# Optimization experiments

Measured on AMD Instinct MI355X. Metric: run time of the kernel, lower is better.

The kernel has to match this reference:

```python
import jax, jax.numpy as jnp
import numpy as np

def setup_inputs() -> dict:
    key = jax.random.key(0)
    ks = jax.random.split(key, 8)
    B, C, H, W = 4, 64, 64, 64
    Cr = C // 8
    s = 1.0 / np.sqrt(C)
    return {
        "x": jax.random.normal(ks[0], (B, C, H, W), jnp.float32),
        "wq": jax.random.normal(ks[1], (Cr, C), jnp.float32) * s,
        "bq": jax.random.normal(ks[2], (Cr,), jnp.float32) * 0.01,
        "wk": jax.random.normal(ks[3], (Cr, C), jnp.float32) * s,
        "bk": jax.random.normal(ks[4], (Cr,), jnp.float32) * 0.01,
        "wv": jax.random.normal(ks[5], (C, C), jnp.float32) * s,
        "bv": jax.random.normal(ks[6], (C,), jnp.float32) * 0.01,
        "gamma": jax.random.normal(ks[7], (1,), jnp.float32) * 0.1,
    }

def reference(x, wq, bq, wk, bk, wv, bv, gamma):
    B, C, H, W = x.shape
    N = H * W
    xf = x.reshape(B, C, N)  # 1x1 conv == pointwise linear over channel dim
    q = jnp.einsum("oc,bcn->bno", wq, xf) + bq[None, None, :]   # (B, N, Cr)
    k = jnp.einsum("oc,bcn->bon", wk, xf) + bk[None, :, None]   # (B, Cr, N)
    v = jnp.einsum("oc,bcn->bon", wv, xf) + bv[None, :, None]   # (B, C, N)
    attn = jnp.einsum("bno,bom->bnm", q, k)                     # (B, N, N)
    attn = jax.nn.softmax(attn, axis=-1)
    out = jnp.einsum("bcm,bnm->bcn", v, attn)                   # (B, C, N)
    out = out.reshape(B, C, H, W)
    return x + gamma[0] * out
```

## Files before the change

### kernel.cpp

```cpp
#include <hip/hip_runtime.h>

#define BB 4
#define CC 64
#define NN 4096

typedef __attribute__((ext_vector_type(8)))  short short8;
typedef __attribute__((ext_vector_type(4)))  short short4v;
typedef __attribute__((ext_vector_type(4)))  float f32x4;
typedef __attribute__((ext_vector_type(16))) float f32x16;
typedef unsigned short u16;

#define QWS_ELEMS (BB * NN * 8)

__device__ inline u16 f2bf(float x) {
    unsigned u = __float_as_uint(x);
    u = (u + 0x7fffu + ((u >> 16) & 1u)) >> 16;
    return (u16)u;
}
__device__ inline unsigned pack2rne(float a, float b) {
    return (unsigned)f2bf(a) | ((unsigned)f2bf(b) << 16);
}
__device__ inline unsigned permpack(float lo, float hi) {
    return __builtin_amdgcn_perm(__float_as_uint(hi), __float_as_uint(lo), 0x07060302);
}

__device__ inline void barrier_lgkm() {
    asm volatile("s_waitcnt lgkmcnt(0)\n\ts_barrier" ::: "memory");
}

union SH8 {
    short8 s;
    struct Halves { short4v lo, hi; } h;
    uint4 u;
};

__global__ __launch_bounds__(512) void proj_kernel(
    const float* __restrict__ x,
    const float* __restrict__ wq, const float* __restrict__ bq,
    const float* __restrict__ wk, const float* __restrict__ bk,
    const float* __restrict__ wv, const float* __restrict__ bv,
    u16* __restrict__ ws_u)
{
    u16* qws = ws_u;
    u16* kws = ws_u + QWS_ELEMS;
    u16* vws = ws_u + 2 * QWS_ELEMS;

    const int y   = blockIdx.y;
    const int pix = blockIdx.x * 512 + threadIdx.x;
    const int b   = pix >> 12;
    const int n   = pix & (NN - 1);
    const float* xb = x + ((size_t)b << 18) + n;

    if (y < 8) {
        const int v0 = y << 3;
        float av[8];
#pragma unroll
        for (int i = 0; i < 8; ++i) av[i] = bv[v0 + i];
#pragma unroll 8
        for (int c = 0; c < CC; ++c) {
            const float xv = xb[(size_t)c << 12];
#pragma unroll
            for (int i = 0; i < 8; ++i)
                av[i] += wv[(v0 + i) * CC + c] * xv;
        }
#pragma unroll
        for (int i = 0; i < 8; ++i)
            vws[(((size_t)((b << 6) + v0 + i)) << 12) + n] = f2bf(av[i]);
    } else {
        float aq[8], ak[8];
#pragma unroll
        for (int i = 0; i < 8; ++i) { aq[i] = bq[i]; ak[i] = bk[i]; }
#pragma unroll 8
        for (int c = 0; c < CC; ++c) {
            const float xv = xb[(size_t)c << 12];
#pragma unroll
            for (int i = 0; i < 8; ++i) {
                aq[i] += wq[i * CC + c] * xv;
                ak[i] += wk[i * CC + c] * xv;
            }
        }
        uint4 qp, kp;
        qp.x = pack2rne(aq[0], aq[1]); qp.y = pack2rne(aq[2], aq[3]);
        qp.z = pack2rne(aq[4], aq[5]); qp.w = pack2rne(aq[6], aq[7]);
        kp.x = pack2rne(ak[0], ak[1]); kp.y = pack2rne(ak[2], ak[3]);
        kp.z = pack2rne(ak[4], ak[5]); kp.w = pack2rne(ak[6], ak[7]);
        *(uint4*)&qws[(size_t)pix * 8] = qp;
        *(uint4*)&kws[(size_t)pix * 8] = kp;
    }
}

__global__ __launch_bounds__(512) void attn_kernel(
    const float* __restrict__ x, const float* __restrict__ gamma,
    const u16* __restrict__ ws_u, float* __restrict__ out)
{
    const u16* qws = ws_u;
    const u16* kws = ws_u + QWS_ELEMS;
    const u16* vws = ws_u + 2 * QWS_ELEMS;

    __shared__ __align__(16) char smem[34816 + 1024 + 256];
    u16*   v_t    = (u16*)smem;
    float* eb     = (float*)smem;
    float* l_part = (float*)(smem + 34816);
    float* l_inv  = (float*)(smem + 34816 + 1024);

    const int tid  = threadIdx.x;
    const int w    = tid >> 6;
    const int lane = tid & 63;
    const int l31  = lane & 31;
    const int lh   = lane >> 5;
    const int mh   = w >> 1;
    const int qh   = w & 1;

    const int b  = blockIdx.y;
    const int qb = blockIdx.x << 6;
    const int bN = b << 12;

    short8 qf = {0,0,0,0,0,0,0,0};
    short8 kf = {0,0,0,0,0,0,0,0};
    if (lane < 32) {
        qf = *(const short8*)(qws + (size_t)(bN + qb + (qh << 5) + l31) * 8);
        kf = *(const short8*)(kws + (size_t)(bN + (mh << 5) + l31) * 8);
    }
    short8 kn = kf;

    const int c_st = tid >> 3;
    const int o_st = (tid & 7) << 3;
    const u16* vgr = vws + (((size_t)((b << 6) + c_st)) << 12) + o_st;
    const int st0  = c_st * 132 + o_st;

    SH8 va0, va1, vb0, vb1;
    va0.s = *(const short8*)(vgr);
    va1.s = *(const short8*)(vgr + 64);
    *(short4v*)&v_t[st0]      = va0.h.lo;
    *(short4v*)&v_t[st0 + 4]  = va0.h.hi;
    *(short4v*)&v_t[st0 + 64] = va1.h.lo;
    *(short4v*)&v_t[st0 + 68] = va1.h.hi;
    va0.s = *(const short8*)(vgr + 128);
    va1.s = *(const short8*)(vgr + 192);

    const int rA = l31 * 132;
    const int rB = (32 + l31) * 132;
    const int mb = (mh << 5) + (lh << 2);

    f32x16 z16, acc0, acc1;
#pragma unroll
    for (int r = 0; r < 16; ++r) { z16[r] = 0.f; acc0[r] = 0.f; acc1[r] = 0.f; }
    float ls = 0.f;

    barrier_lgkm();

#pragma unroll 2
    for (int it = 0; it < 32; ++it) {
        const int buf = (it & 1) * (CC * 132);
        const int nxt = ((it + 1) & 31) << 7;
        const int nx2 = ((it + 2) & 31) << 7;

        vb0.s = *(const short8*)(vgr + nx2);
        vb1.s = *(const short8*)(vgr + nx2 + 64);
        if (lane < 32)
            kn = *(const short8*)(kws + (size_t)(bN + nxt + (mh << 5) + l31) * 8);

        f32x16 d = __builtin_amdgcn_mfma_f32_32x32x16_bf16(kf, qf, z16, 0, 0, 0);

        float p[16];
#pragma unroll
        for (int r = 0; r < 16; ++r) p[r] = __expf(d[r]);
        float s0 = 0.f, s1 = 0.f;
#pragma unroll
        for (int r = 0; r < 8; ++r) { s0 += p[2 * r]; s1 += p[2 * r + 1]; }
        ls += s0 + s1;

        SH8 A0, A1;
        A0.u.x = permpack(p[0],  p[1]);  A0.u.y = permpack(p[2],  p[3]);
        A0.u.z = permpack(p[4],  p[5]);  A0.u.w = permpack(p[6],  p[7]);
        A1.u.x = permpack(p[8],  p[9]);  A1.u.y = permpack(p[10], p[11]);
        A1.u.z = permpack(p[12], p[13]); A1.u.w = permpack(p[14], p[15]);

        SH8 B00, B01, B10, B11;
        B00.h.lo = *(const short4v*)&v_t[buf + rA + mb];
        B00.h.hi = *(const short4v*)&v_t[buf + rA + mb + 8];
        B01.h.lo = *(const short4v*)&v_t[buf + rB + mb];
        B01.h.hi = *(const short4v*)&v_t[buf + rB + mb + 8];
        B10.h.lo = *(const short4v*)&v_t[buf + rA + mb + 16];
        B10.h.hi = *(const short4v*)&v_t[buf + rA + mb + 24];
        B11.h.lo = *(const short4v*)&v_t[buf + rB + mb + 16];
        B11.h.hi = *(const short4v*)&v_t[buf + rB + mb + 24];

        acc0 = __builtin_amdgcn_mfma_f32_32x32x16_bf16(A0.s, B00.s, acc0, 0, 0, 0);
        acc1 = __builtin_amdgcn_mfma_f32_32x32x16_bf16(A0.s, B01.s, acc1, 0, 0, 0);
        acc0 = __builtin_amdgcn_mfma_f32_32x32x16_bf16(A1.s, B10.s, acc0, 0, 0, 0);
        acc1 = __builtin_amdgcn_mfma_f32_32x32x16_bf16(A1.s, B11.s, acc1, 0, 0, 0);

        const int ob = (CC * 132) - buf;
        *(short4v*)&v_t[ob + st0]      = va0.h.lo;
        *(short4v*)&v_t[ob + st0 + 4]  = va0.h.hi;
        *(short4v*)&v_t[ob + st0 + 64] = va1.h.lo;
        *(short4v*)&v_t[ob + st0 + 68] = va1.h.hi;
        va0 = vb0; va1 = vb1;
        kf = kn;

        barrier_lgkm();
    }

    float lt = ls + __shfl_xor(ls, 32, 64);
    if (lane < 32) l_part[(mh * 2 + qh) * 32 + l31] = lt;
    __syncthreads();
    if (w < 2 && lane < 32) {
        float s = l_part[(0 * 2 + qh) * 32 + l31] + l_part[(1 * 2 + qh) * 32 + l31]
                + l_part[(2 * 2 + qh) * 32 + l31] + l_part[(3 * 2 + qh) * 32 + l31];
        l_inv[qh * 32 + l31] = 1.0f / s;
    }

    if (mh >= 2) {
        float* e0 = &eb[(((mh - 2) << 2) + (qh << 1) + 0) * 1088 + lane * 17];
        float* e1 = &eb[(((mh - 2) << 2) + (qh << 1) + 1) * 1088 + lane * 17];
#pragma unroll
        for (int r = 0; r < 16; ++r) { e0[r] = acc0[r]; e1[r] = acc1[r]; }
    }
    __syncthreads();
    if (mh < 2) {
        const float* e0 = &eb[((mh << 2) + (qh << 1) + 0) * 1088 + lane * 17];
        const float* e1 = &eb[((mh << 2) + (qh << 1) + 1) * 1088 + lane * 17];
#pragma unroll
        for (int r = 0; r < 16; ++r) { acc0[r] += e0[r]; acc1[r] += e1[r]; }
    }
    __syncthreads();
    if (mh == 1) {
        float* e0 = &eb[((qh << 1) + 0) * 1088 + lane * 17];
        float* e1 = &eb[((qh << 1) + 1) * 1088 + lane * 17];
#pragma unroll
        for (int r = 0; r < 16; ++r) { e0[r] = acc0[r]; e1[r] = acc1[r]; }
    }
    __syncthreads();
    if (w < 2) {
        const float* e0 = &eb[((qh << 1) + 0) * 1088 + lane * 17];
        const float* e1 = &eb[((qh << 1) + 1) * 1088 + lane * 17];
#pragma unroll
        for (int r = 0; r < 16; ++r) { acc0[r] += e0[r]; acc1[r] += e1[r]; }

        f32x4 li[4];
#pragma unroll
        for (int k = 0; k < 4; ++k)
            li[k] = *(const f32x4*)&l_inv[qh * 32 + (k << 3) + (lh << 2)];
        const float g = gamma[0];
#pragma unroll
        for (int ch = 0; ch < 2; ++ch) {
            const int c = (ch << 5) + l31;
            const f32x16 a = ch ? acc1 : acc0;
            const size_t rowb = (((size_t)((b << 6) + c)) << 12) + qb + (qh << 5);
#pragma unroll
            for (int k = 0; k < 4; ++k) {
                const int q0 = (k << 3) + (lh << 2);
                const float4 xv = *(const float4*)&x[rowb + q0];
                float4 o;
                o.x = xv.x + g * a[4 * k + 0] * li[k][0];
                o.y = xv.y + g * a[4 * k + 1] * li[k][1];
                o.z = xv.z + g * a[4 * k + 2] * li[k][2];
                o.w = xv.w + g * a[4 * k + 3] * li[k][3];
                *(float4*)&out[rowb + q0] = o;
            }
        }
    }
}

extern "C" void kernel_launch(void* const* d_in, const int* in_sizes, int n_in,
                              void* d_out, int out_size, void* d_ws, size_t ws_size,
                              hipStream_t stream)
{
    const float* x     = (const float*)d_in[0];
    const float* wq    = (const float*)d_in[1];
    const float* bq    = (const float*)d_in[2];
    const float* wk    = (const float*)d_in[3];
    const float* bk    = (const float*)d_in[4];
    const float* wv    = (const float*)d_in[5];
    const float* bv    = (const float*)d_in[6];
    const float* gamma = (const float*)d_in[7];
    u16*   ws  = (u16*)d_ws;
    float* out = (float*)d_out;

    hipLaunchKernelGGL(proj_kernel, dim3(BB * NN / 512, 9), dim3(512), 0, stream,
                       x, wq, bq, wk, bk, wv, bv, ws);
    hipLaunchKernelGGL(attn_kernel, dim3(NN / 64, BB), dim3(512), 0, stream,
                       x, gamma, ws, out);
}
```

Before: 104.2 us.

## Balance projection work across blocks and stage attention epilogue through shared memory

The projection kernel drops its ninth, heavier y-slice that computed all of Q and K. Each of the 8 slices now computes 8 V channels plus 2 Q or K channels, which balances work per block and removes the long-tail block row. In the attention kernel, gamma is folded into the softmax normalizer. The final scaled output is written to shared memory, then all 512 threads do the residual add with coalesced float4 loads and stores, instead of only two waves writing strided rows. The price is an extra barrier and more shared-memory traffic in the epilogue, plus 4-byte partial stores into the Q/K buffers.

```diff
diff --git a/kernel.cpp b/kernel.cpp
--- a/kernel.cpp
+++ b/kernel.cpp
@@ -51,42 +51,31 @@
     const int n   = pix & (NN - 1);
     const float* xb = x + ((size_t)b << 18) + n;
 
-    if (y < 8) {
-        const int v0 = y << 3;
-        float av[8];
-#pragma unroll
-        for (int i = 0; i < 8; ++i) av[i] = bv[v0 + i];
+    const int v0  = y << 3;
+    const int isq = (y < 4) ? 1 : 0;
+    const int qc0 = (y & 3) << 1;
+    const float* wj = isq ? wq : wk;
+    const float* bj = isq ? bq : bk;
+
+    float av[8];
+    float a0 = bj[qc0], a1 = bj[qc0 + 1];
+#pragma unroll
+    for (int i = 0; i < 8; ++i) av[i] = bv[v0 + i];
 #pragma unroll 8
-        for (int c = 0; c < CC; ++c) {
-            const float xv = xb[(size_t)c << 12];
-#pragma unroll
-            for (int i = 0; i < 8; ++i)
-                av[i] += wv[(v0 + i) * CC + c] * xv;
-        }
+    for (int c = 0; c < CC; ++c) {
+        const float xv = xb[(size_t)c << 12];
 #pragma unroll
         for (int i = 0; i < 8; ++i)
-            vws[(((size_t)((b << 6) + v0 + i)) << 12) + n] = f2bf(av[i]);
-    } else {
-        float aq[8], ak[8];
-#pragma unroll
-        for (int i = 0; i < 8; ++i) { aq[i] = bq[i]; ak[i] = bk[i]; }
-#pragma unroll 8
-        for (int c = 0; c < CC; ++c) {
-            const float xv = xb[(size_t)c << 12];
-#pragma unroll
-            for (int i = 0; i < 8; ++i) {
-                aq[i] += wq[i * CC + c] * xv;
-                ak[i] += wk[i * CC + c] * xv;
-            }
-        }
-        uint4 qp, kp;
-        qp.x = pack2rne(aq[0], aq[1]); qp.y = pack2rne(aq[2], aq[3]);
-        qp.z = pack2rne(aq[4], aq[5]); qp.w = pack2rne(aq[6], aq[7]);
-        kp.x = pack2rne(ak[0], ak[1]); kp.y = pack2rne(ak[2], ak[3]);
-        kp.z = pack2rne(ak[4], ak[5]); kp.w = pack2rne(ak[6], ak[7]);
-        *(uint4*)&qws[(size_t)pix * 8] = qp;
-        *(uint4*)&kws[(size_t)pix * 8] = kp;
-    }
+            av[i] += wv[(v0 + i) * CC + c] * xv;
+        a0 += wj[qc0 * CC + c] * xv;
+        a1 += wj[(qc0 + 1) * CC + c] * xv;
+    }
+#pragma unroll
+    for (int i = 0; i < 8; ++i)
+        vws[(((size_t)((b << 6) + v0 + i)) << 12) + n] = f2bf(av[i]);
+
+    u16* dst = (isq ? qws : kws) + (size_t)pix * 8 + qc0;
+    *(unsigned*)dst = pack2rne(a0, a1);
 }
 
 __global__ __launch_bounds__(512) void attn_kernel(
@@ -100,6 +89,7 @@
     __shared__ __align__(16) char smem[34816 + 1024 + 256];
     u16*   v_t    = (u16*)smem;
     float* eb     = (float*)smem;
+    float* eb2    = (float*)smem;
     float* l_part = (float*)(smem + 34816);
     float* l_inv  = (float*)(smem + 34816 + 1024);
 
@@ -208,7 +198,7 @@
     if (w < 2 && lane < 32) {
         float s = l_part[(0 * 2 + qh) * 32 + l31] + l_part[(1 * 2 + qh) * 32 + l31]
                 + l_part[(2 * 2 + qh) * 32 + l31] + l_part[(3 * 2 + qh) * 32 + l31];
-        l_inv[qh * 32 + l31] = 1.0f / s;
+        l_inv[qh * 32 + l31] = gamma[0] / s;
     }
 
     if (mh >= 2) {
@@ -237,29 +227,43 @@
         const float* e1 = &eb[((qh << 1) + 1) * 1088 + lane * 17];
 #pragma unroll
         for (int r = 0; r < 16; ++r) { acc0[r] += e0[r]; acc1[r] += e1[r]; }
-
+    }
+    __syncthreads();
+
+    if (w < 2) {
         f32x4 li[4];
 #pragma unroll
         for (int k = 0; k < 4; ++k)
             li[k] = *(const f32x4*)&l_inv[qh * 32 + (k << 3) + (lh << 2)];
-        const float g = gamma[0];
 #pragma unroll
         for (int ch = 0; ch < 2; ++ch) {
             const int c = (ch << 5) + l31;
             const f32x16 a = ch ? acc1 : acc0;
-            const size_t rowb = (((size_t)((b << 6) + c)) << 12) + qb + (qh << 5);
+            float* er = eb2 + c * 69 + (qh << 5) + (lh << 2);
 #pragma unroll
             for (int k = 0; k < 4; ++k) {
-                const int q0 = (k << 3) + (lh << 2);
-                const float4 xv = *(const float4*)&x[rowb + q0];
-                float4 o;
-                o.x = xv.x + g * a[4 * k + 0] * li[k][0];
-                o.y = xv.y + g * a[4 * k + 1] * li[k][1];
-                o.z = xv.z + g * a[4 * k + 2] * li[k][2];
-                o.w = xv.w + g * a[4 * k + 3] * li[k][3];
-                *(float4*)&out[rowb + q0] = o;
+#pragma unroll
+                for (int r = 0; r < 4; ++r)
+                    er[(k << 3) + r] = a[4 * k + r] * li[k][r];
             }
         }
+    }
+    __syncthreads();
+
+    {
+        const int c2 = tid >> 3;
+        const int qo = (tid & 7) << 3;
+        const float* er = eb2 + c2 * 69 + qo;
+        const size_t rowb = (((size_t)((b << 6) + c2)) << 12) + qb + qo;
+        const float4 x0 = *(const float4*)&x[rowb];
+        const float4 x1 = *(const float4*)&x[rowb + 4];
+        float4 o0, o1;
+        o0.x = x0.x + er[0]; o0.y = x0.y + er[1];
+        o0.z = x0.z + er[2]; o0.w = x0.w + er[3];
+        o1.x = x1.x + er[4]; o1.y = x1.y + er[5];
+        o1.z = x1.z + er[6]; o1.w = x1.w + er[7];
+        *(float4*)&out[rowb]     = o0;
+        *(float4*)&out[rowb + 4] = o1;
     }
 }
 
@@ -278,7 +282,7 @@
     u16*   ws  = (u16*)d_ws;
     float* out = (float*)d_out;
 
-    hipLaunchKernelGGL(proj_kernel, dim3(BB * NN / 512, 9), dim3(512), 0, stream,
+    hipLaunchKernelGGL(proj_kernel, dim3(BB * NN / 512, 8), dim3(512), 0, stream,
                        x, wq, bq, wk, bk, wv, bv, ws);
     hipLaunchKernelGGL(attn_kernel, dim3(NN / 64, BB), dim3(512), 0, stream,
                        x, gamma, ws, out);
```

After: 99.89 us. 4.1% less time.
